# Optimization experiments

Hardware: AMD Instinct MI355X
Metric: run time of the kernel (lower is better)

## Reference

```python
import jax, jax.numpy as jnp
import numpy as np

D_MODEL = 1024; D_STATE = 128; EXPAND = 2; HEADDIM = 64
D_INNER = EXPAND * D_MODEL; NHEADS = D_INNER // HEADDIM; PF = 2  # param_factor for complex
BATCH = 2; SEQ = 2048
DT_MIN = 0.001; DT_MAX = 0.1


def setup_inputs() -> dict:
    key = jax.random.key(0)
    k = jax.random.split(key, 10)
    u = jax.random.normal(k[0], (BATCH, SEQ, D_MODEL), jnp.float32)
    in_proj_w = jax.random.normal(k[1], (2 * D_INNER, D_MODEL), jnp.float32) * (D_MODEL ** -0.5)
    dt_projs_weight = jax.random.normal(k[2], (NHEADS, D_INNER), jnp.float32) * 0.02
    dt_projs_bias = (jax.random.uniform(k[3], (NHEADS,), jnp.float32)
                     * (np.log(DT_MAX) - np.log(DT_MIN)) + np.log(DT_MIN)).astype(jnp.float32)
    x_proj_w = jax.random.normal(k[4], (NHEADS * (1 + 2 * D_STATE * PF), D_INNER), jnp.float32) * (D_INNER ** -0.5)
    A = jnp.stack([-jax.random.uniform(k[5], (NHEADS, D_STATE), dtype=jnp.float32),
                   jax.random.normal(k[6], (NHEADS, D_STATE), jnp.float32) * 0.1], axis=-1)  # (H,N,2)
    D = jnp.ones((NHEADS,), jnp.float32)
    norm_B_w = jnp.ones((2 * D_STATE,), jnp.float32)
    norm_C_w = jnp.ones((2 * D_STATE,), jnp.float32)
    out_proj_w = jax.random.normal(k[7], (D_MODEL, D_INNER), jnp.float32) * (D_INNER ** -0.5)
    return {"u": u, "in_proj_w": in_proj_w, "dt_projs_weight": dt_projs_weight,
            "dt_projs_bias": dt_projs_bias, "x_proj_w": x_proj_w, "A": A, "D": D,
            "norm_B_w": norm_B_w, "norm_C_w": norm_C_w, "out_proj_w": out_proj_w}


def _rms_norm(x, w, eps=1e-6):
    return x * jax.lax.rsqrt(jnp.mean(x * x, axis=-1, keepdims=True) + eps) * w


def reference(u, in_proj_w, dt_projs_weight, dt_projs_bias, x_proj_w, A, D,
              norm_B_w, norm_C_w, out_proj_w):
    Bsz, L, _ = u.shape
    xz = u @ in_proj_w.T                        # (B,L,2*d_inner)
    x, z = jnp.split(xz, 2, axis=-1)
    x = jax.nn.silu(x)                          # (B,L,d_inner)
    dt = jax.nn.softplus(x @ dt_projs_weight.T + dt_projs_bias)  # (B,L,H)

    BCp = (x @ x_proj_w.T).reshape(Bsz, L, NHEADS, -1)
    BC = BCp[..., :2 * D_STATE * PF].reshape(Bsz, L, NHEADS, 2, D_STATE, PF)
    Bn = _rms_norm(BC[..., 0, :, :].reshape(Bsz, L, NHEADS, D_STATE * PF), norm_B_w)
    Cn = _rms_norm(BC[..., 1, :, :].reshape(Bsz, L, NHEADS, D_STATE * PF), norm_C_w)
    Bn = Bn.reshape(Bsz, L, NHEADS, D_STATE, PF)
    Cn = Cn.reshape(Bsz, L, NHEADS, D_STATE, PF)
    Bc = jax.lax.complex(Bn[..., 0], Bn[..., 1])  # (B,L,H,N) complex64
    Cc = jax.lax.complex(Cn[..., 0], Cn[..., 1])
    Ac = jax.lax.complex(A[..., 0], A[..., 1])    # (H,N) complex64

    xh = x.reshape(Bsz, L, NHEADS, HEADDIM)
    x_sum = xh.sum(axis=-1)                       # (B,L,H) -- kernel sums x_t over headdim
    zt = Ac[None, None] * (0.5 * dt)[..., None]   # (B,L,H,N) complex: A*dt/2
    den = 1.0 - zt
    abar = (1.0 + zt) / den                       # bilinear (Tustin) discretization
    u_in = Bc * ((dt * x_sum)[..., None] / den)   # Bbar * sum(x_t)

    def step(h, inp):
        a, b = inp
        h = a * h + b
        return h, h

    h0 = jnp.zeros((Bsz, NHEADS, D_STATE), jnp.complex64)
    _, hs = jax.lax.scan(step, h0, (jnp.swapaxes(abar, 0, 1), jnp.swapaxes(u_in, 0, 1)))
    hs = jnp.swapaxes(hs, 0, 1)                   # (B,L,H,N)
    y_red = jnp.real(Cc * hs).sum(axis=-1)        # (B,L,H), Re(C*h) reduced over state
    y = (xh * (y_red + D)[..., None]).reshape(Bsz, L, D_INNER)
    y = y * jax.nn.silu(z)
    return y @ out_proj_w.T
```

## Files before the change

kernel.cpp:

```cpp
#include <hip/hip_runtime.h>

#define BATCH   2
#define SEQ     2048
#define DMODEL  1024
#define DINNER  2048
#define NHEADS  32
#define HEADDIM 64
#define DSTATE  128
#define BLTOT   (BATCH * SEQ)
#define NCHUNK  32
#define CHUNK   64

#define OFF_UB   0ull
#define OFF_WXZ  8388608ull
#define OFF_WBC  16777216ull
#define OFF_WOUT 83886080ull
#define OFF_XB   88080384ull
#define OFF_YB   104857600ull
#define OFF_BC   121634816ull
#define OFF_SZ   255852544ull
#define OFF_DT   272629760ull
#define OFF_XS   273154048ull
#define OFF_YR   273678336ull
#define OFF_CA   274202624ull
#define OFF_CS   276299776ull
#define OFF_HI   278396928ull
#define OFF_SS   280494080ull

typedef __attribute__((ext_vector_type(8))) short bf16x8;
typedef __attribute__((ext_vector_type(4))) float f32x4;

__device__ __forceinline__ float b2f(unsigned short u) {
    return __uint_as_float(((unsigned)u) << 16);
}
__device__ __forceinline__ unsigned short f2b(float f) {
    unsigned x = __float_as_uint(f);
    unsigned r = (x + 0x7fffu + ((x >> 16) & 1u)) >> 16;
    return (unsigned short)r;
}
__device__ __forceinline__ float silu_f(float v) {
    return v / (1.0f + __expf(-v));
}
__device__ __forceinline__ float softplus_f(float v) {
    return (v > 20.0f) ? v : log1pf(__expf(v));
}

__device__ __forceinline__ void gload_lds16(const void* g, void* l) {
    __builtin_amdgcn_global_load_lds(
        (const __attribute__((address_space(1))) unsigned int*)g,
        (__attribute__((address_space(3))) unsigned int*)l, 16, 0, 0);
}

__global__ __launch_bounds__(256) void conv_all_kernel(
    const float* __restrict__ u, const float* __restrict__ ipw,
    const float* __restrict__ opw, const float* __restrict__ xpw,
    unsigned short* __restrict__ u_b, unsigned short* __restrict__ w_xz,
    unsigned short* __restrict__ w_out, unsigned short* __restrict__ w_bc) {
    long idx = (long)blockIdx.x * 256 + threadIdx.x;
    if (idx >= 2621440L) {
        long e = (idx - 2621440L) * 4;
        long c = e >> 11, k = e & 2047;
        const float* s = xpw + ((c >> 9) * 513 + (c & 511)) * 2048 + k;
        float4 v = *(const float4*)s;
        ushort4 o = {f2b(v.x), f2b(v.y), f2b(v.z), f2b(v.w)};
        *(ushort4*)&w_bc[e] = o;
        return;
    }
    const float* src;
    unsigned short* dst;
    long i;
    if (idx < 1048576L)      { src = u;   dst = u_b;   i = idx; }
    else if (idx < 2097152L) { src = ipw; dst = w_xz;  i = idx - 1048576L; }
    else                     { src = opw; dst = w_out; i = idx - 2097152L; }
    float4 v = *(const float4*)&src[i * 4];
    ushort4 o = {f2b(v.x), f2b(v.y), f2b(v.z), f2b(v.w)};
    *(ushort4*)&dst[i * 4] = o;
}

template <int KTOT, int KLEN, int MODE>
__device__ __forceinline__ void gemm_body(
    const unsigned short* __restrict__ A, const unsigned short* __restrict__ B,
    void* __restrict__ C0, void* __restrict__ C1, float* __restrict__ C2,
    float* __restrict__ ssbuf, int N, int koff) {
    __shared__ short ldsA[128 * 32];
    __shared__ short ldsB[128 * 32];
    int tid = threadIdx.x;
    int row0 = blockIdx.y * 128, col0 = blockIdx.x * 128;
    int lane = tid & 63, wave = tid >> 6;
    int wrow = (wave >> 1) * 64, wcol = (wave & 1) * 64;
    int m = lane & 15, quad = lane >> 4;

    f32x4 acc[4][4];
#pragma unroll
    for (int i = 0; i < 4; ++i)
#pragma unroll
        for (int j = 0; j < 4; ++j) acc[i][j] = (f32x4){0.f, 0.f, 0.f, 0.f};

    int r = tid >> 2, c8 = (tid & 3) * 8;
    const unsigned short* Ag = A + (size_t)(row0 + r) * KTOT + koff + c8;
    const unsigned short* Bg = B + (size_t)(col0 + r) * KTOT + koff + c8;
    short* la = ldsA + tid * 8;
    short* lb = ldsB + tid * 8;

    for (int k0 = 0; k0 < KLEN; k0 += 32) {
        gload_lds16(Ag + k0, la);
        gload_lds16(Ag + (size_t)64 * KTOT + k0, la + 2048);
        gload_lds16(Bg + k0, lb);
        gload_lds16(Bg + (size_t)64 * KTOT + k0, lb + 2048);
        __syncthreads();
        bf16x8 af[4], bfr[4];
#pragma unroll
        for (int i = 0; i < 4; ++i)
            af[i] = *(const bf16x8*)&ldsA[(wrow + i * 16 + m) * 32 + quad * 8];
#pragma unroll
        for (int j = 0; j < 4; ++j)
            bfr[j] = *(const bf16x8*)&ldsB[(wcol + j * 16 + m) * 32 + quad * 8];
#pragma unroll
        for (int i = 0; i < 4; ++i)
#pragma unroll
            for (int j = 0; j < 4; ++j)
                acc[i][j] = __builtin_amdgcn_mfma_f32_16x16x32_bf16(
                    af[i], bfr[j], acc[i][j], 0, 0, 0);
        __syncthreads();
    }

    if (MODE == 1) {
        bool isx = (col0 < DINNER);
        if (isx) {
            int head = (col0 + wcol) >> 6;
            float ssum[4][4];
#pragma unroll
            for (int i = 0; i < 4; ++i)
#pragma unroll
                for (int reg = 0; reg < 4; ++reg) ssum[i][reg] = 0.f;
#pragma unroll
            for (int i = 0; i < 4; ++i)
#pragma unroll
                for (int reg = 0; reg < 4; ++reg) {
                    int row = row0 + wrow + i * 16 + quad * 4 + reg;
#pragma unroll
                    for (int j = 0; j < 4; ++j) {
                        int col = col0 + wcol + j * 16 + m;
                        float s = silu_f(acc[i][j][reg]);
                        ((unsigned short*)C0)[(size_t)row * DINNER + col] = f2b(s);
                        ssum[i][reg] += s;
                    }
                }
#pragma unroll
            for (int i = 0; i < 4; ++i)
#pragma unroll
                for (int reg = 0; reg < 4; ++reg) {
                    float s = ssum[i][reg];
                    s += __shfl_xor(s, 1);
                    s += __shfl_xor(s, 2);
                    s += __shfl_xor(s, 4);
                    s += __shfl_xor(s, 8);
                    if (m == 0) {
                        int row = row0 + wrow + i * 16 + quad * 4 + reg;
                        C2[(size_t)row * NHEADS + head] = s;
                    }
                }
        } else {
#pragma unroll
            for (int i = 0; i < 4; ++i)
#pragma unroll
                for (int reg = 0; reg < 4; ++reg) {
                    int row = row0 + wrow + i * 16 + quad * 4 + reg;
#pragma unroll
                    for (int j = 0; j < 4; ++j) {
                        int col = col0 + wcol + j * 16 + m - DINNER;
                        float s = silu_f(acc[i][j][reg]);
                        ((unsigned short*)C1)[(size_t)row * DINNER + col] = f2b(s);
                    }
                }
        }
    } else if (MODE == 2) {
        int g = (col0 + wcol) >> 8;
        float ssq[4][4];
#pragma unroll
        for (int i = 0; i < 4; ++i)
#pragma unroll
            for (int reg = 0; reg < 4; ++reg) ssq[i][reg] = 0.f;
#pragma unroll
        for (int i = 0; i < 4; ++i)
#pragma unroll
            for (int reg = 0; reg < 4; ++reg) {
                int row = row0 + wrow + i * 16 + quad * 4 + reg;
#pragma unroll
                for (int j = 0; j < 4; ++j) {
                    int col = col0 + wcol + j * 16 + m;
                    float v = acc[i][j][reg];
                    ((unsigned short*)C0)[(size_t)row * N + col] = f2b(v);
                    ssq[i][reg] += v * v;
                }
            }
#pragma unroll
        for (int i = 0; i < 4; ++i)
#pragma unroll
            for (int reg = 0; reg < 4; ++reg) {
                float s = ssq[i][reg];
                s += __shfl_xor(s, 1);
                s += __shfl_xor(s, 2);
                s += __shfl_xor(s, 4);
                s += __shfl_xor(s, 8);
                if (m == 0) {
                    int row = row0 + wrow + i * 16 + quad * 4 + reg;
                    atomicAdd(&ssbuf[(size_t)row * 64 + g], s);
                }
            }
    } else {
#pragma unroll
        for (int i = 0; i < 4; ++i)
#pragma unroll
            for (int reg = 0; reg < 4; ++reg) {
                int row = row0 + wrow + i * 16 + quad * 4 + reg;
#pragma unroll
                for (int j = 0; j < 4; ++j) {
                    int col = col0 + wcol + j * 16 + m;
                    atomicAdd(&((float*)C0)[(size_t)row * N + col],
                              acc[i][j][reg]);
                }
            }
    }
}

__global__ __launch_bounds__(256) void gemm_xz_kernel(
    const unsigned short* __restrict__ A, const unsigned short* __restrict__ B,
    void* C0, void* C1, float* C2) {
    gemm_body<1024, 1024, 1>(A, B, C0, C1, C2, nullptr, 4096, 0);
}
__global__ __launch_bounds__(256) void gemm_bc_kernel(
    const unsigned short* __restrict__ A, const unsigned short* __restrict__ B,
    void* C0, float* ssbuf) {
    gemm_body<2048, 2048, 2>(A, B, C0, nullptr, nullptr, ssbuf, 16384, 0);
}
__global__ __launch_bounds__(256) void gemm_out_kernel(
    const unsigned short* __restrict__ A, const unsigned short* __restrict__ B,
    void* C0) {
    gemm_body<2048, 512, 3>(A, B, C0, nullptr, nullptr, nullptr, 1024,
                            blockIdx.z * 512);
}

__global__ __launch_bounds__(256) void dt_kernel(
    const unsigned short* __restrict__ x, const float* __restrict__ dtw,
    const float* __restrict__ dtb, float* __restrict__ dt) {
    __shared__ float xs[16][132];
    __shared__ float ws[32][132];
    int r0 = blockIdx.x * 16;
    int t = threadIdx.x;
    int lrow = t >> 4, lc8 = (t & 15) * 8;
    int lh = t >> 3, lc16 = (t & 7) * 16;
    int row = t >> 4, h0 = t & 15;
    float acc0 = 0.f, acc1 = 0.f;

    for (int kc = 0; kc < DINNER; kc += 128) {
        ushort4 a = *(const ushort4*)&x[(size_t)(r0 + lrow) * DINNER + kc + lc8];
        ushort4 b = *(const ushort4*)&x[(size_t)(r0 + lrow) * DINNER + kc + lc8 + 4];
        xs[lrow][lc8 + 0] = b2f(a.x); xs[lrow][lc8 + 1] = b2f(a.y);
        xs[lrow][lc8 + 2] = b2f(a.z); xs[lrow][lc8 + 3] = b2f(a.w);
        xs[lrow][lc8 + 4] = b2f(b.x); xs[lrow][lc8 + 5] = b2f(b.y);
        xs[lrow][lc8 + 6] = b2f(b.z); xs[lrow][lc8 + 7] = b2f(b.w);
#pragma unroll
        for (int q = 0; q < 4; ++q) {
            float4 w = *(const float4*)&dtw[(size_t)lh * DINNER + kc + lc16 + q * 4];
            *(float4*)&ws[lh][lc16 + q * 4] = w;
        }
        __syncthreads();
#pragma unroll
        for (int k = 0; k < 128; k += 4) {
            float4 xv = *(const float4*)&xs[row][k];
            float4 w0 = *(const float4*)&ws[h0][k];
            float4 w1 = *(const float4*)&ws[h0 + 16][k];
            acc0 += xv.x * w0.x + xv.y * w0.y + xv.z * w0.z + xv.w * w0.w;
            acc1 += xv.x * w1.x + xv.y * w1.y + xv.z * w1.z + xv.w * w1.w;
        }
        __syncthreads();
    }
    dt[(size_t)(r0 + row) * NHEADS + h0]      = softplus_f(acc0 + dtb[h0]);
    dt[(size_t)(r0 + row) * NHEADS + h0 + 16] = softplus_f(acc1 + dtb[h0 + 16]);
}

__device__ __forceinline__ void coefs(
    float ar, float ai, float dtv, float xsv, float Br, float Bi,
    float& abr, float& abi, float& ur, float& ui) {
    float hd = 0.5f * dtv;
    float ztr = ar * hd, zti = ai * hd;
    float denr = 1.0f - ztr;
    float s2 = 1.0f / (denr * denr + zti * zti);
    float invr = denr * s2, invi = zti * s2;
    float opr = 1.0f + ztr;
    abr = opr * invr - zti * invi;
    abi = opr * invi + zti * invr;
    float coef = dtv * xsv;
    float cr = coef * invr, ci = coef * invi;
    ur = Br * cr - Bi * ci;
    ui = Br * ci + Bi * cr;
}

__global__ __launch_bounds__(64) void scan_pass1(
    const unsigned short* __restrict__ bc, const float* __restrict__ dt,
    const float* __restrict__ xsum, const float* __restrict__ A,
    const float* __restrict__ wB, const float* __restrict__ ssbuf,
    float2* __restrict__ cA, float2* __restrict__ cS) {
    int blk = blockIdx.x;
    int bh = blk >> 5, c = blk & (NCHUNK - 1);
    int b = bh >> 5, h = bh & 31;
    int t = threadIdx.x;
    float4 av = *(const float4*)&A[(h * DSTATE + 2 * t) * 2];
    float4 wv = *(const float4*)&wB[4 * t];
    int l0 = c * CHUNK;
    const unsigned short* base = bc + ((size_t)(b * SEQ + l0)) * 16384 + h * 512;
    const float* dtp = dt + (b * SEQ + l0) * NHEADS + h;
    const float* xsp = xsum + (b * SEQ + l0) * NHEADS + h;
    const float* ssp = ssbuf + (size_t)(b * SEQ + l0) * 64 + 2 * h;

    float pr0 = 1.f, pi0 = 0.f, sr0 = 0.f, si0 = 0.f;
    float pr1 = 1.f, pi1 = 0.f, sr1 = 0.f, si1 = 0.f;
    for (int l = 0; l < CHUNK; ++l) {
        uint2 bw = *(const uint2*)&base[(size_t)l * 16384 + 4 * t];
        float scale = rsqrtf(ssp[l * 64] * (1.0f / 256.0f) + 1e-6f);
        float Br0 = b2f((unsigned short)(bw.x & 0xffff)) * scale * wv.x;
        float Bi0 = b2f((unsigned short)(bw.x >> 16)) * scale * wv.y;
        float Br1 = b2f((unsigned short)(bw.y & 0xffff)) * scale * wv.z;
        float Bi1 = b2f((unsigned short)(bw.y >> 16)) * scale * wv.w;
        float dtv = dtp[l * NHEADS], xsv = xsp[l * NHEADS];
        float abr, abi, ur, ui;
        coefs(av.x, av.y, dtv, xsv, Br0, Bi0, abr, abi, ur, ui);
        float ns = abr * sr0 - abi * si0 + ur;
        float nsi = abr * si0 + abi * sr0 + ui;
        sr0 = ns; si0 = nsi;
        float np = abr * pr0 - abi * pi0;
        float npi = abr * pi0 + abi * pr0;
        pr0 = np; pi0 = npi;
        coefs(av.z, av.w, dtv, xsv, Br1, Bi1, abr, abi, ur, ui);
        ns = abr * sr1 - abi * si1 + ur;
        nsi = abr * si1 + abi * sr1 + ui;
        sr1 = ns; si1 = nsi;
        np = abr * pr1 - abi * pi1;
        npi = abr * pi1 + abi * pr1;
        pr1 = np; pi1 = npi;
    }
    size_t idx = ((size_t)bh * NCHUNK + c) * DSTATE + 2 * t;
    *(float4*)&cA[idx] = (float4){pr0, pi0, pr1, pi1};
    *(float4*)&cS[idx] = (float4){sr0, si0, sr1, si1};
}

__global__ __launch_bounds__(128) void scan_fixup(
    const float2* __restrict__ cA, const float2* __restrict__ cS,
    float2* __restrict__ hin) {
    int bh = blockIdx.x;
    int n = threadIdx.x;
    float hr = 0.f, hi = 0.f;
    for (int c = 0; c < NCHUNK; ++c) {
        size_t idx = ((size_t)bh * NCHUNK + c) * DSTATE + n;
        hin[idx] = {hr, hi};
        float2 a = cA[idx];
        float2 s = cS[idx];
        float nhr = a.x * hr - a.y * hi + s.x;
        float nhi = a.x * hi + a.y * hr + s.y;
        hr = nhr; hi = nhi;
    }
}

__global__ __launch_bounds__(64) void scan_pass2(
    const unsigned short* __restrict__ bc, const float* __restrict__ dt,
    const float* __restrict__ xsum, const float* __restrict__ A,
    const float* __restrict__ wB, const float* __restrict__ wC,
    const float* __restrict__ ssbuf, const float2* __restrict__ hin,
    float* __restrict__ yredp) {
    int blk = blockIdx.x;
    int bh = blk >> 5, c = blk & (NCHUNK - 1);
    int b = bh >> 5, h = bh & 31;
    int t = threadIdx.x;
    float4 av = *(const float4*)&A[(h * DSTATE + 2 * t) * 2];
    float4 wbv = *(const float4*)&wB[4 * t];
    float4 wcv = *(const float4*)&wC[4 * t];
    int l0 = c * CHUNK;
    const unsigned short* base = bc + ((size_t)(b * SEQ + l0)) * 16384 + h * 512;
    const float* dtp = dt + (b * SEQ + l0) * NHEADS + h;
    const float* xsp = xsum + (b * SEQ + l0) * NHEADS + h;
    const float* ssp = ssbuf + (size_t)(b * SEQ + l0) * 64 + 2 * h;
    float* yp = yredp + (size_t)(b * SEQ + l0) * NHEADS + h;

    float4 h0v = *(const float4*)&hin[((size_t)bh * NCHUNK + c) * DSTATE + 2 * t];
    float hr0 = h0v.x, hi0 = h0v.y, hr1 = h0v.z, hi1 = h0v.w;

    for (int l = 0; l < CHUNK; ++l) {
        uint2 bw = *(const uint2*)&base[(size_t)l * 16384 + 4 * t];
        uint2 cw = *(const uint2*)&base[(size_t)l * 16384 + 256 + 4 * t];
        float sB = rsqrtf(ssp[l * 64 + 0] * (1.0f / 256.0f) + 1e-6f);
        float sC = rsqrtf(ssp[l * 64 + 1] * (1.0f / 256.0f) + 1e-6f);
        float Br0 = b2f((unsigned short)(bw.x & 0xffff)) * sB * wbv.x;
        float Bi0 = b2f((unsigned short)(bw.x >> 16)) * sB * wbv.y;
        float Br1 = b2f((unsigned short)(bw.y & 0xffff)) * sB * wbv.z;
        float Bi1 = b2f((unsigned short)(bw.y >> 16)) * sB * wbv.w;
        float Cr0 = b2f((unsigned short)(cw.x & 0xffff)) * sC * wcv.x;
        float Ci0 = b2f((unsigned short)(cw.x >> 16)) * sC * wcv.y;
        float Cr1 = b2f((unsigned short)(cw.y & 0xffff)) * sC * wcv.z;
        float Ci1 = b2f((unsigned short)(cw.y >> 16)) * sC * wcv.w;
        float dtv = dtp[l * NHEADS], xsv = xsp[l * NHEADS];
        float abr, abi, ur, ui;
        coefs(av.x, av.y, dtv, xsv, Br0, Bi0, abr, abi, ur, ui);
        float nhr = abr * hr0 - abi * hi0 + ur;
        float nhi = abr * hi0 + abi * hr0 + ui;
        hr0 = nhr; hi0 = nhi;
        coefs(av.z, av.w, dtv, xsv, Br1, Bi1, abr, abi, ur, ui);
        nhr = abr * hr1 - abi * hi1 + ur;
        nhi = abr * hi1 + abi * hr1 + ui;
        hr1 = nhr; hi1 = nhi;
        float y = Cr0 * hr0 - Ci0 * hi0 + Cr1 * hr1 - Ci1 * hi1;
#pragma unroll
        for (int off = 1; off < 64; off <<= 1) y += __shfl_xor(y, off);
        if (t == 0) yp[(size_t)l * NHEADS] = y;
    }
}

__global__ __launch_bounds__(256) void yfuse_kernel(
    const unsigned short* __restrict__ x, const unsigned short* __restrict__ sz,
    const float* __restrict__ yredp, const float* __restrict__ Dv,
    unsigned short* __restrict__ y) {
    int i = (blockIdx.x * 256 + threadIdx.x) * 4;
    int r = i >> 11;
    int k = i & (DINNER - 1);
    int h = k >> 6;
    float yr = yredp[(size_t)r * NHEADS + h] + Dv[h];
    ushort4 xv = *(const ushort4*)&x[i];
    ushort4 zv = *(const ushort4*)&sz[i];
    ushort4 o = {f2b(b2f(xv.x) * yr * b2f(zv.x)),
                 f2b(b2f(xv.y) * yr * b2f(zv.y)),
                 f2b(b2f(xv.z) * yr * b2f(zv.z)),
                 f2b(b2f(xv.w) * yr * b2f(zv.w))};
    *(ushort4*)&y[i] = o;
}

extern "C" void kernel_launch(void* const* d_in, const int* in_sizes, int n_in,
                              void* d_out, int out_size, void* d_ws, size_t ws_size,
                              hipStream_t stream) {
    const float* u   = (const float*)d_in[0];
    const float* ipw = (const float*)d_in[1];
    const float* dtw = (const float*)d_in[2];
    const float* dtb = (const float*)d_in[3];
    const float* xpw = (const float*)d_in[4];
    const float* A   = (const float*)d_in[5];
    const float* Dv  = (const float*)d_in[6];
    const float* wB  = (const float*)d_in[7];
    const float* wC  = (const float*)d_in[8];
    const float* opw = (const float*)d_in[9];
    float* out = (float*)d_out;
    char* ws = (char*)d_ws;

    unsigned short* u_b   = (unsigned short*)(ws + OFF_UB);
    unsigned short* w_xz  = (unsigned short*)(ws + OFF_WXZ);
    unsigned short* w_bc  = (unsigned short*)(ws + OFF_WBC);
    unsigned short* w_out = (unsigned short*)(ws + OFF_WOUT);
    unsigned short* x_b   = (unsigned short*)(ws + OFF_XB);
    unsigned short* y_b   = (unsigned short*)(ws + OFF_YB);
    unsigned short* bc    = (unsigned short*)(ws + OFF_BC);
    unsigned short* sz    = (unsigned short*)(ws + OFF_SZ);
    float* dt    = (float*)(ws + OFF_DT);
    float* xsum  = (float*)(ws + OFF_XS);
    float* yredp = (float*)(ws + OFF_YR);
    float2* cA   = (float2*)(ws + OFF_CA);
    float2* cS   = (float2*)(ws + OFF_CS);
    float2* hin  = (float2*)(ws + OFF_HI);
    float* ssbuf = (float*)(ws + OFF_SS);

    hipMemsetAsync(ssbuf, 0, (size_t)BLTOT * 64 * 4, stream);
    hipMemsetAsync(out, 0, (size_t)BLTOT * DMODEL * 4, stream);

    conv_all_kernel<<<43008, 256, 0, stream>>>(u, ipw, opw, xpw,
                                               u_b, w_xz, w_out, w_bc);

    gemm_xz_kernel<<<dim3(32, 32), 256, 0, stream>>>(u_b, w_xz, x_b, sz, xsum);
    dt_kernel<<<BLTOT / 16, 256, 0, stream>>>(x_b, dtw, dtb, dt);
    gemm_bc_kernel<<<dim3(128, 32), 256, 0, stream>>>(x_b, w_bc, bc, ssbuf);

    scan_pass1<<<BATCH * NHEADS * NCHUNK, 64, 0, stream>>>(
        bc, dt, xsum, A, wB, ssbuf, cA, cS);
    scan_fixup<<<BATCH * NHEADS, 128, 0, stream>>>(cA, cS, hin);
    scan_pass2<<<BATCH * NHEADS * NCHUNK, 64, 0, stream>>>(
        bc, dt, xsum, A, wB, wC, ssbuf, hin, yredp);

    yfuse_kernel<<<BLTOT * DINNER / 4 / 256, 256, 0, stream>>>(
        x_b, sz, yredp, Dv, y_b);
    gemm_out_kernel<<<dim3(8, 32, 4), 256, 0, stream>>>(y_b, w_out, out);
}
```

Baseline: 884.6 us.

## Store BC head-major, compute RMS sums separately, replace atomics with split-K partial buffers

The BC GEMM now writes its output in a head-major layout (head, row, 512), so each scan block reads contiguous 1 KB rows instead of rows strided by 32 KB. The RMS sum-of-squares atomics in the GEMM epilogue are replaced by a separate ss_kernel that reduces over the new layout. The out-projection drops its 4-way split-K with float atomics and memset, and instead writes two partial buffers that a small kernel adds together. The dt kernel is also reshaped to 8 rows per block with one head per thread. In exchange there are two extra launches and extra traffic for the partial buffers and the sum-of-squares pass.

```diff
diff --git a/kernel.cpp b/kernel.cpp
--- a/kernel.cpp
+++ b/kernel.cpp
@@ -26,6 +26,8 @@
 #define OFF_CS   276299776ull
 #define OFF_HI   278396928ull
 #define OFF_SS   280494080ull
+#define OFF_P0   281542656ull
+#define OFF_P1   298319872ull
 
 typedef __attribute__((ext_vector_type(8))) short bf16x8;
 typedef __attribute__((ext_vector_type(4))) float f32x4;
@@ -81,7 +83,7 @@
 __device__ __forceinline__ void gemm_body(
     const unsigned short* __restrict__ A, const unsigned short* __restrict__ B,
     void* __restrict__ C0, void* __restrict__ C1, float* __restrict__ C2,
-    float* __restrict__ ssbuf, int N, int koff) {
+    int N, int koff) {
     __shared__ short ldsA[128 * 32];
     __shared__ short ldsB[128 * 32];
     int tid = threadIdx.x;
@@ -175,50 +177,29 @@
                 }
         }
     } else if (MODE == 2) {
-        int g = (col0 + wcol) >> 8;
-        float ssq[4][4];
-#pragma unroll
-        for (int i = 0; i < 4; ++i)
-#pragma unroll
-            for (int reg = 0; reg < 4; ++reg) ssq[i][reg] = 0.f;
+        int hH = (col0 + wcol) >> 9;
+        int w0 = (col0 + wcol) & 511;
 #pragma unroll
         for (int i = 0; i < 4; ++i)
 #pragma unroll
             for (int reg = 0; reg < 4; ++reg) {
                 int row = row0 + wrow + i * 16 + quad * 4 + reg;
+                unsigned short* dst =
+                    (unsigned short*)C0 + ((size_t)hH * BLTOT + row) * 512 + w0;
+#pragma unroll
+                for (int j = 0; j < 4; ++j)
+                    dst[j * 16 + m] = f2b(acc[i][j][reg]);
+            }
+    } else {
+#pragma unroll
+        for (int i = 0; i < 4; ++i)
+#pragma unroll
+            for (int reg = 0; reg < 4; ++reg) {
+                int row = row0 + wrow + i * 16 + quad * 4 + reg;
 #pragma unroll
                 for (int j = 0; j < 4; ++j) {
                     int col = col0 + wcol + j * 16 + m;
-                    float v = acc[i][j][reg];
-                    ((unsigned short*)C0)[(size_t)row * N + col] = f2b(v);
-                    ssq[i][reg] += v * v;
-                }
-            }
-#pragma unroll
-        for (int i = 0; i < 4; ++i)
-#pragma unroll
-            for (int reg = 0; reg < 4; ++reg) {
-                float s = ssq[i][reg];
-                s += __shfl_xor(s, 1);
-                s += __shfl_xor(s, 2);
-                s += __shfl_xor(s, 4);
-                s += __shfl_xor(s, 8);
-                if (m == 0) {
-                    int row = row0 + wrow + i * 16 + quad * 4 + reg;
-                    atomicAdd(&ssbuf[(size_t)row * 64 + g], s);
-                }
-            }
-    } else {
-#pragma unroll
-        for (int i = 0; i < 4; ++i)
-#pragma unroll
-            for (int reg = 0; reg < 4; ++reg) {
-                int row = row0 + wrow + i * 16 + quad * 4 + reg;
-#pragma unroll
-                for (int j = 0; j < 4; ++j) {
-                    int col = col0 + wcol + j * 16 + m;
-                    atomicAdd(&((float*)C0)[(size_t)row * N + col],
-                              acc[i][j][reg]);
+                    ((float*)C0)[(size_t)row * N + col] = acc[i][j][reg];
                 }
             }
     }
@@ -227,39 +208,47 @@
 __global__ __launch_bounds__(256) void gemm_xz_kernel(
     const unsigned short* __restrict__ A, const unsigned short* __restrict__ B,
     void* C0, void* C1, float* C2) {
-    gemm_body<1024, 1024, 1>(A, B, C0, C1, C2, nullptr, 4096, 0);
+    gemm_body<1024, 1024, 1>(A, B, C0, C1, C2, 4096, 0);
 }
 __global__ __launch_bounds__(256) void gemm_bc_kernel(
     const unsigned short* __restrict__ A, const unsigned short* __restrict__ B,
-    void* C0, float* ssbuf) {
-    gemm_body<2048, 2048, 2>(A, B, C0, nullptr, nullptr, ssbuf, 16384, 0);
+    void* C0) {
+    gemm_body<2048, 2048, 2>(A, B, C0, nullptr, nullptr, 16384, 0);
 }
 __global__ __launch_bounds__(256) void gemm_out_kernel(
     const unsigned short* __restrict__ A, const unsigned short* __restrict__ B,
-    void* C0) {
-    gemm_body<2048, 512, 3>(A, B, C0, nullptr, nullptr, nullptr, 1024,
-                            blockIdx.z * 512);
+    float* P0, float* P1) {
+    float* dst = blockIdx.z ? P1 : P0;
+    gemm_body<2048, 1024, 0>(A, B, dst, nullptr, nullptr, 1024,
+                             blockIdx.z * 1024);
+}
+
+__global__ __launch_bounds__(256) void yout_reduce_kernel(
+    const float* __restrict__ p0, const float* __restrict__ p1,
+    float* __restrict__ out) {
+    int i = (blockIdx.x * 256 + threadIdx.x) * 4;
+    float4 a = *(const float4*)&p0[i];
+    float4 b = *(const float4*)&p1[i];
+    float4 o = {a.x + b.x, a.y + b.y, a.z + b.z, a.w + b.w};
+    *(float4*)&out[i] = o;
 }
 
 __global__ __launch_bounds__(256) void dt_kernel(
     const unsigned short* __restrict__ x, const float* __restrict__ dtw,
     const float* __restrict__ dtb, float* __restrict__ dt) {
-    __shared__ float xs[16][132];
+    __shared__ float xs[8][132];
     __shared__ float ws[32][132];
-    int r0 = blockIdx.x * 16;
+    int r0 = blockIdx.x * 8;
     int t = threadIdx.x;
-    int lrow = t >> 4, lc8 = (t & 15) * 8;
+    int lrow = t >> 5, lc4 = (t & 31) * 4;
     int lh = t >> 3, lc16 = (t & 7) * 16;
-    int row = t >> 4, h0 = t & 15;
-    float acc0 = 0.f, acc1 = 0.f;
+    int row = t >> 5, h = t & 31;
+    float acc = 0.f;
 
     for (int kc = 0; kc < DINNER; kc += 128) {
-        ushort4 a = *(const ushort4*)&x[(size_t)(r0 + lrow) * DINNER + kc + lc8];
-        ushort4 b = *(const ushort4*)&x[(size_t)(r0 + lrow) * DINNER + kc + lc8 + 4];
-        xs[lrow][lc8 + 0] = b2f(a.x); xs[lrow][lc8 + 1] = b2f(a.y);
-        xs[lrow][lc8 + 2] = b2f(a.z); xs[lrow][lc8 + 3] = b2f(a.w);
-        xs[lrow][lc8 + 4] = b2f(b.x); xs[lrow][lc8 + 5] = b2f(b.y);
-        xs[lrow][lc8 + 6] = b2f(b.z); xs[lrow][lc8 + 7] = b2f(b.w);
+        ushort4 a = *(const ushort4*)&x[(size_t)(r0 + lrow) * DINNER + kc + lc4];
+        xs[lrow][lc4 + 0] = b2f(a.x); xs[lrow][lc4 + 1] = b2f(a.y);
+        xs[lrow][lc4 + 2] = b2f(a.z); xs[lrow][lc4 + 3] = b2f(a.w);
 #pragma unroll
         for (int q = 0; q < 4; ++q) {
             float4 w = *(const float4*)&dtw[(size_t)lh * DINNER + kc + lc16 + q * 4];
@@ -269,15 +258,31 @@
 #pragma unroll
         for (int k = 0; k < 128; k += 4) {
             float4 xv = *(const float4*)&xs[row][k];
-            float4 w0 = *(const float4*)&ws[h0][k];
-            float4 w1 = *(const float4*)&ws[h0 + 16][k];
-            acc0 += xv.x * w0.x + xv.y * w0.y + xv.z * w0.z + xv.w * w0.w;
-            acc1 += xv.x * w1.x + xv.y * w1.y + xv.z * w1.z + xv.w * w1.w;
+            float4 wv = *(const float4*)&ws[h][k];
+            acc += xv.x * wv.x + xv.y * wv.y + xv.z * wv.z + xv.w * wv.w;
         }
         __syncthreads();
     }
-    dt[(size_t)(r0 + row) * NHEADS + h0]      = softplus_f(acc0 + dtb[h0]);
-    dt[(size_t)(r0 + row) * NHEADS + h0 + 16] = softplus_f(acc1 + dtb[h0 + 16]);
+    dt[(size_t)(r0 + row) * NHEADS + h] = softplus_f(acc + dtb[h]);
+}
+
+__global__ __launch_bounds__(256) void ss_kernel(
+    const unsigned short* __restrict__ bct, float* __restrict__ ss) {
+    int wgid = blockIdx.x * 4 + (threadIdx.x >> 6);
+    int lane = threadIdx.x & 63;
+    const unsigned short* p = bct + (size_t)wgid * 512 + lane * 8;
+    ushort4 a = *(const ushort4*)p;
+    ushort4 b = *(const ushort4*)(p + 4);
+    float f0 = b2f(a.x), f1 = b2f(a.y), f2 = b2f(a.z), f3 = b2f(a.w);
+    float f4 = b2f(b.x), f5 = b2f(b.y), f6 = b2f(b.z), f7 = b2f(b.w);
+    float s = f0 * f0 + f1 * f1 + f2 * f2 + f3 * f3 +
+              f4 * f4 + f5 * f5 + f6 * f6 + f7 * f7;
+    s += __shfl_xor(s, 1);
+    s += __shfl_xor(s, 2);
+    s += __shfl_xor(s, 4);
+    s += __shfl_xor(s, 8);
+    s += __shfl_xor(s, 16);
+    if ((lane & 31) == 0) ss[(size_t)wgid * 2 + (lane >> 5)] = s;
 }
 
 __device__ __forceinline__ void coefs(
@@ -298,9 +303,9 @@
 }
 
 __global__ __launch_bounds__(64) void scan_pass1(
-    const unsigned short* __restrict__ bc, const float* __restrict__ dt,
+    const unsigned short* __restrict__ bct, const float* __restrict__ dt,
     const float* __restrict__ xsum, const float* __restrict__ A,
-    const float* __restrict__ wB, const float* __restrict__ ssbuf,
+    const float* __restrict__ wB, const float* __restrict__ ss,
     float2* __restrict__ cA, float2* __restrict__ cS) {
     int blk = blockIdx.x;
     int bh = blk >> 5, c = blk & (NCHUNK - 1);
@@ -309,16 +314,17 @@
     float4 av = *(const float4*)&A[(h * DSTATE + 2 * t) * 2];
     float4 wv = *(const float4*)&wB[4 * t];
     int l0 = c * CHUNK;
-    const unsigned short* base = bc + ((size_t)(b * SEQ + l0)) * 16384 + h * 512;
+    size_t rbase = (size_t)h * BLTOT + b * SEQ + l0;
+    const unsigned short* base = bct + rbase * 512;
+    const float* ssp = ss + rbase * 2;
     const float* dtp = dt + (b * SEQ + l0) * NHEADS + h;
     const float* xsp = xsum + (b * SEQ + l0) * NHEADS + h;
-    const float* ssp = ssbuf + (size_t)(b * SEQ + l0) * 64 + 2 * h;
 
     float pr0 = 1.f, pi0 = 0.f, sr0 = 0.f, si0 = 0.f;
     float pr1 = 1.f, pi1 = 0.f, sr1 = 0.f, si1 = 0.f;
     for (int l = 0; l < CHUNK; ++l) {
-        uint2 bw = *(const uint2*)&base[(size_t)l * 16384 + 4 * t];
-        float scale = rsqrtf(ssp[l * 64] * (1.0f / 256.0f) + 1e-6f);
+        uint2 bw = *(const uint2*)&base[(size_t)l * 512 + 4 * t];
+        float scale = rsqrtf(ssp[l * 2] * (1.0f / 256.0f) + 1e-6f);
         float Br0 = b2f((unsigned short)(bw.x & 0xffff)) * scale * wv.x;
         float Bi0 = b2f((unsigned short)(bw.x >> 16)) * scale * wv.y;
         float Br1 = b2f((unsigned short)(bw.y & 0xffff)) * scale * wv.z;
@@ -363,10 +369,10 @@
 }
 
 __global__ __launch_bounds__(64) void scan_pass2(
-    const unsigned short* __restrict__ bc, const float* __restrict__ dt,
+    const unsigned short* __restrict__ bct, const float* __restrict__ dt,
     const float* __restrict__ xsum, const float* __restrict__ A,
     const float* __restrict__ wB, const float* __restrict__ wC,
-    const float* __restrict__ ssbuf, const float2* __restrict__ hin,
+    const float* __restrict__ ss, const float2* __restrict__ hin,
     float* __restrict__ yredp) {
     int blk = blockIdx.x;
     int bh = blk >> 5, c = blk & (NCHUNK - 1);
@@ -376,20 +382,21 @@
     float4 wbv = *(const float4*)&wB[4 * t];
     float4 wcv = *(const float4*)&wC[4 * t];
     int l0 = c * CHUNK;
-    const unsigned short* base = bc + ((size_t)(b * SEQ + l0)) * 16384 + h * 512;
+    size_t rbase = (size_t)h * BLTOT + b * SEQ + l0;
+    const unsigned short* base = bct + rbase * 512;
+    const float* ssp = ss + rbase * 2;
     const float* dtp = dt + (b * SEQ + l0) * NHEADS + h;
     const float* xsp = xsum + (b * SEQ + l0) * NHEADS + h;
-    const float* ssp = ssbuf + (size_t)(b * SEQ + l0) * 64 + 2 * h;
     float* yp = yredp + (size_t)(b * SEQ + l0) * NHEADS + h;
 
     float4 h0v = *(const float4*)&hin[((size_t)bh * NCHUNK + c) * DSTATE + 2 * t];
     float hr0 = h0v.x, hi0 = h0v.y, hr1 = h0v.z, hi1 = h0v.w;
 
     for (int l = 0; l < CHUNK; ++l) {
-        uint2 bw = *(const uint2*)&base[(size_t)l * 16384 + 4 * t];
-        uint2 cw = *(const uint2*)&base[(size_t)l * 16384 + 256 + 4 * t];
-        float sB = rsqrtf(ssp[l * 64 + 0] * (1.0f / 256.0f) + 1e-6f);
-        float sC = rsqrtf(ssp[l * 64 + 1] * (1.0f / 256.0f) + 1e-6f);
+        uint2 bw = *(const uint2*)&base[(size_t)l * 512 + 4 * t];
+        uint2 cw = *(const uint2*)&base[(size_t)l * 512 + 256 + 4 * t];
+        float sB = rsqrtf(ssp[l * 2 + 0] * (1.0f / 256.0f) + 1e-6f);
+        float sC = rsqrtf(ssp[l * 2 + 1] * (1.0f / 256.0f) + 1e-6f);
         float Br0 = b2f((unsigned short)(bw.x & 0xffff)) * sB * wbv.x;
         float Bi0 = b2f((unsigned short)(bw.x >> 16)) * sB * wbv.y;
         float Br1 = b2f((unsigned short)(bw.y & 0xffff)) * sB * wbv.z;
@@ -455,7 +462,7 @@
     unsigned short* w_out = (unsigned short*)(ws + OFF_WOUT);
     unsigned short* x_b   = (unsigned short*)(ws + OFF_XB);
     unsigned short* y_b   = (unsigned short*)(ws + OFF_YB);
-    unsigned short* bc    = (unsigned short*)(ws + OFF_BC);
+    unsigned short* bct   = (unsigned short*)(ws + OFF_BC);
     unsigned short* sz    = (unsigned short*)(ws + OFF_SZ);
     float* dt    = (float*)(ws + OFF_DT);
     float* xsum  = (float*)(ws + OFF_XS);
@@ -464,24 +471,25 @@
     float2* cS   = (float2*)(ws + OFF_CS);
     float2* hin  = (float2*)(ws + OFF_HI);
     float* ssbuf = (float*)(ws + OFF_SS);
-
-    hipMemsetAsync(ssbuf, 0, (size_t)BLTOT * 64 * 4, stream);
-    hipMemsetAsync(out, 0, (size_t)BLTOT * DMODEL * 4, stream);
+    float* p0    = (float*)(ws + OFF_P0);
+    float* p1    = (float*)(ws + OFF_P1);
 
     conv_all_kernel<<<43008, 256, 0, stream>>>(u, ipw, opw, xpw,
                                                u_b, w_xz, w_out, w_bc);
 
     gemm_xz_kernel<<<dim3(32, 32), 256, 0, stream>>>(u_b, w_xz, x_b, sz, xsum);
-    dt_kernel<<<BLTOT / 16, 256, 0, stream>>>(x_b, dtw, dtb, dt);
-    gemm_bc_kernel<<<dim3(128, 32), 256, 0, stream>>>(x_b, w_bc, bc, ssbuf);
+    dt_kernel<<<BLTOT / 8, 256, 0, stream>>>(x_b, dtw, dtb, dt);
+    gemm_bc_kernel<<<dim3(128, 32), 256, 0, stream>>>(x_b, w_bc, bct);
+    ss_kernel<<<NHEADS * BLTOT / 4, 256, 0, stream>>>(bct, ssbuf);
 
     scan_pass1<<<BATCH * NHEADS * NCHUNK, 64, 0, stream>>>(
-        bc, dt, xsum, A, wB, ssbuf, cA, cS);
+        bct, dt, xsum, A, wB, ssbuf, cA, cS);
     scan_fixup<<<BATCH * NHEADS, 128, 0, stream>>>(cA, cS, hin);
     scan_pass2<<<BATCH * NHEADS * NCHUNK, 64, 0, stream>>>(
-        bc, dt, xsum, A, wB, wC, ssbuf, hin, yredp);
+        bct, dt, xsum, A, wB, wC, ssbuf, hin, yredp);
 
     yfuse_kernel<<<BLTOT * DINNER / 4 / 256, 256, 0, stream>>>(
         x_b, sz, yredp, Dv, y_b);
-    gemm_out_kernel<<<dim3(8, 32, 4), 256, 0, stream>>>(y_b, w_out, out);
-}
+    gemm_out_kernel<<<dim3(8, 32, 2), 256, 0, stream>>>(y_b, w_out, p0, p1);
+    yout_reduce_kernel<<<BLTOT * DMODEL / 4 / 256, 256, 0, stream>>>(p0, p1, out);
+}
```

New measurement: 832.5 us. -5.9%, faster.
